# Kernel optimization log

Measured on AMD Instinct MI355X. Metric: run time of the kernel, lower is better.

Reference implementation:

```python
import jax, jax.numpy as jnp
import numpy as np

LRELU_SLOPE = 0.1  # correlate_operator uses F.leaky_relu_(corr, 0.1)


def _conv2d(x, w, b):
    # x: [B,Ci,H,W], w: [Co,Ci,kh,kw], stride 1, padding SAME (=padding=1 for 3x3)
    y = jax.lax.conv_general_dilated(x, w, (1, 1), 'SAME',
                                     dimension_numbers=('NCHW', 'OIHW', 'NCHW'))
    return y + b[None, :, None, None]


def correlate(x1, x2):
    # spatial_correlation_sample(x1, x2, kernel_size=3, patch_size=1, stride=1,
    # padding=1): with patch_size=1 the only displacement is (0,0), so the cost
    # volume is a 3x3 window sum of the per-pixel channel dot product.
    # Then divided by C and leaky_relu(0.1) as in correlate_operator.
    prod = jnp.sum(x1 * x2, axis=1, keepdims=True)  # [B,1,H,W]
    box = jnp.ones((1, 1, 3, 3), prod.dtype)
    corr = jax.lax.conv_general_dilated(prod, box, (1, 1), 'SAME',
                                        dimension_numbers=('NCHW', 'OIHW', 'NCHW'))
    corr = corr / x1.shape[1]
    return jnp.where(corr > 0, corr, LRELU_SLOPE * corr)


def deform_conv2d(x, offset, w):
    # mmcv DeformConv2d: kernel 3x3, stride 1, pad 1, dilation 1, deform_groups=1,
    # bias=False. offset: [B, 2*kh*kw, H, W], per kernel tap k: (dy_k, dx_k).
    B, Cin, H, W = x.shape
    O, _, kh, kw = w.shape
    K = kh * kw
    off = offset.reshape(B, K, 2, H, W)
    dy, dx = off[:, :, 0], off[:, :, 1]  # [B,K,H,W]
    ky, kx = jnp.meshgrid(jnp.arange(kh), jnp.arange(kw), indexing='ij')
    # sampling position: p + p_k + offset_k (pad=1 cancels the kernel-center shift)
    y = jnp.arange(H, dtype=x.dtype)[None, None, :, None] \
        + (ky.reshape(-1) - kh // 2).astype(x.dtype)[None, :, None, None] + dy
    xx = jnp.arange(W, dtype=x.dtype)[None, None, None, :] \
        + (kx.reshape(-1) - kw // 2).astype(x.dtype)[None, :, None, None] + dx
    y0 = jnp.floor(y)
    x0 = jnp.floor(xx)
    wy = (y - y0)[:, None]   # [B,1,K,H,W]
    wx = (xx - x0)[:, None]
    y0i = y0.astype(jnp.int32)
    x0i = x0.astype(jnp.int32)
    xf = x.reshape(B, Cin, H * W)

    def gather(yi, xi):
        valid = (yi >= 0) & (yi < H) & (xi >= 0) & (xi < W)  # zero padding outside
        idx = jnp.clip(yi, 0, H - 1) * W + jnp.clip(xi, 0, W - 1)
        v = jnp.take_along_axis(xf, idx.reshape(B, 1, K * H * W), axis=2)
        return v.reshape(B, Cin, K, H, W) * valid.astype(x.dtype)[:, None]

    v00 = gather(y0i, x0i)
    v01 = gather(y0i, x0i + 1)
    v10 = gather(y0i + 1, x0i)
    v11 = gather(y0i + 1, x0i + 1)
    samp = (v00 * (1 - wy) * (1 - wx) + v01 * (1 - wy) * wx
            + v10 * wy * (1 - wx) + v11 * wy * wx)  # [B,Cin,K,H,W]
    return jnp.einsum('bckhw,ock->bohw', samp, w.reshape(O, Cin, K))


def setup_inputs() -> dict:
    key = jax.random.key(0)
    ks = jax.random.split(key, 10)
    B, C, H, W = 4, 256, 64, 64
    s = 0.02
    return {
        'x_ref': jax.random.normal(ks[0], (B, C, H, W), jnp.float32),
        'x_next': jax.random.normal(ks[1], (B, C, H, W), jnp.float32),
        'w1': jax.random.normal(ks[2], (256, 1, 3, 3), jnp.float32) * s,
        'b1': jax.random.normal(ks[3], (256,), jnp.float32) * s,
        'w2': jax.random.normal(ks[4], (256, 256, 3, 3), jnp.float32) * s,
        'b2': jax.random.normal(ks[5], (256,), jnp.float32) * s,
        'w3': jax.random.normal(ks[6], (18, 256, 3, 3), jnp.float32) * s,
        'b3': jax.random.normal(ks[7], (18,), jnp.float32) * s,
        'w_dcn': jax.random.normal(ks[8], (256, 256, 3, 3), jnp.float32) * s,
        'idx': 4,
    }


def reference(x_ref, x_next, w1, b1, w2, b2, w3, b3, w_dcn, idx):
    # idx=4 -> corr_patch_size=1 (consistent with conv1 in_channels)
    corr = correlate(x_next, x_ref)                      # [B,1,H,W]
    h = jax.nn.relu(_conv2d(corr, w1, b1))               # [B,256,H,W]
    h = jax.nn.relu(_conv2d(h, w2, b2))                  # [B,256,H,W]
    offset = jax.nn.relu(_conv2d(h, w3, b3))             # [B,18,H,W]
    x_ref_cal = jax.nn.relu(deform_conv2d(x_ref, offset, w_dcn))
    return 0.5 * (x_next + x_ref_cal)
```

## Files before the change

kernel.cpp:

```cpp
#include <hip/hip_runtime.h>

typedef __attribute__((ext_vector_type(8))) short short8v;
typedef __attribute__((ext_vector_type(4))) float f32x4;
typedef __attribute__((ext_vector_type(2))) float f32x2;
typedef __attribute__((ext_vector_type(4))) unsigned int u32x4;

constexpr int Bsz = 4;
constexpr int Hh = 64, Wwd = 64;
constexpr int HWp = Hh * Wwd;
constexpr int NPIX = Bsz * HWp;
constexpr int HH = 66;
constexpr int HPIX = HH * HH;
constexpr int Kdim = 2304;
constexpr int NSTEP = 36;

constexpr size_t B_H1H  = 0;
constexpr size_t HALO_BYTES = (size_t)Bsz * HPIX * 256 * 2;
constexpr size_t B_H2H  = B_H1H + HALO_BYTES;
constexpr size_t B_XTH  = B_H2H + HALO_BYTES;
constexpr size_t B_PROD = B_XTH + HALO_BYTES;
constexpr size_t B_OFFP = B_PROD + (size_t)NPIX * 4;
constexpr size_t B_WB2  = B_OFFP + (size_t)NPIX * 32 * 4;
constexpr size_t B_WBD  = B_WB2 + (size_t)256 * Kdim * 2;
constexpr size_t B_WB3  = B_WBD + (size_t)256 * Kdim * 2;

static __device__ __forceinline__ unsigned short f2bf(float f) {
    unsigned u = __builtin_bit_cast(unsigned, f);
    u += 0x7FFFu + ((u >> 16) & 1u);
    return (unsigned short)(u >> 16);
}
static __device__ __forceinline__ unsigned cvt_pk_bf16(float lo, float hi) {
    unsigned r;
    asm("v_cvt_pk_bf16_f32 %0, %1, %2" : "=v"(r) : "v"(lo), "v"(hi));
    return r;
}
static __device__ __forceinline__ f32x2 pk_mul(f32x2 a, f32x2 b) {
    f32x2 d;
    asm("v_pk_mul_f32 %0, %1, %2" : "=v"(d) : "v"(a), "v"(b));
    return d;
}
static __device__ __forceinline__ f32x2 pk_fma(f32x2 a, f32x2 b, f32x2 c) {
    f32x2 d;
    asm("v_pk_fma_f32 %0, %1, %2, %3" : "=v"(d) : "v"(a), "v"(b), "v"(c));
    return d;
}
static __device__ __forceinline__ f32x2 unpack2(unsigned u) {
    f32x2 v;
    v.x = __builtin_bit_cast(float, u << 16);
    v.y = __builtin_bit_cast(float, u & 0xFFFF0000u);
    return v;
}
static __device__ __forceinline__ int swz(int u) {
    return (((u & 7) ^ ((u >> 3) & 7)) << 3);
}

__global__ void k_zero_ring(unsigned short* h1h, unsigned short* h2h, unsigned short* xth,
                            float* prod) {
    int blk = blockIdx.x;
    if (blk >= 3120) {
        unsigned* p = (unsigned*)prod + (size_t)(blk - 3120) * 128 + threadIdx.x;
        *p = 0;
        return;
    }
    int img = blk / 260;
    int rp = blk - img * 260;
    int buf = img >> 2, b = img & 3;
    int y, x;
    if (rp < 66) { y = 0; x = rp; }
    else if (rp < 132) { y = 65; x = rp - 66; }
    else { int s2 = rp - 132; y = 1 + (s2 >> 1); x = (s2 & 1) * 65; }
    unsigned short* base = (buf == 0) ? h1h : (buf == 1) ? h2h : xth;
    unsigned* p = (unsigned*)(base + ((size_t)b * HPIX + y * HH + x) * 256);
    p[threadIdx.x] = 0;
}

__global__ void k_prodx(const float* __restrict__ xr, const float* __restrict__ xn,
                        unsigned short* __restrict__ xth, float* __restrict__ prod) {
    __shared__ float t[32][33];
    __shared__ float red[8][33];
    int b = blockIdx.z;
    int c0 = blockIdx.y * 32;
    int y = blockIdx.x >> 1, x0 = (blockIdx.x & 1) * 32;
    int tx = threadIdx.x, ty = threadIdx.y;
    float part = 0.f;
#pragma unroll
    for (int i = 0; i < 32; i += 8) {
        size_t idx = ((size_t)b * 256 + c0 + ty + i) * HWp + y * Wwd + x0 + tx;
        float vr = xr[idx];
        float vn = xn[idx];
        t[ty + i][tx] = vr;
        part = fmaf(vr, vn, part);
    }
    red[ty][tx] = part;
    __syncthreads();
#pragma unroll
    for (int i = 0; i < 32; i += 8)
        xth[((size_t)b * HPIX + (y + 1) * HH + (x0 + ty + i + 1)) * 256 + c0 + tx] =
            f2bf(t[tx][ty + i]);
    if (ty == 0) {
        float s = red[0][tx] + red[1][tx] + red[2][tx] + red[3][tx] +
                  red[4][tx] + red[5][tx] + red[6][tx] + red[7][tx];
        atomicAdd(&prod[b * HWp + y * Wwd + x0 + tx], s);
    }
}

__global__ __launch_bounds__(256) void k_conv1c(const float* __restrict__ prod,
                                                const float* __restrict__ w1,
                                                const float* __restrict__ b1,
                                                unsigned short* __restrict__ h1h) {
    __shared__ float pp[5][36];
    __shared__ float pt[3][34];
    int px0 = blockIdx.x * 32;
    int b = px0 >> 12, y = (px0 & 4095) >> 6, x0 = px0 & 63;
    int tid = threadIdx.x;
    if (tid < 180) {
        int i = tid / 36, j = tid - i * 36;
        int yy = y - 2 + i, xx = x0 - 2 + j;
        float v = 0.f;
        if (yy >= 0 && yy < Hh && xx >= 0 && xx < Wwd) v = prod[b * HWp + yy * Wwd + xx];
        pp[i][j] = v;
    }
    __syncthreads();
    if (tid < 102) {
        int i = tid / 34, j = tid - i * 34;
        int yy = y - 1 + i, xx = x0 - 1 + j;
        float v = 0.f;
        if (yy >= 0 && yy < Hh && xx >= 0 && xx < Wwd) {
            float s = pp[i][j]     + pp[i][j + 1]     + pp[i][j + 2] +
                      pp[i + 1][j] + pp[i + 1][j + 1] + pp[i + 1][j + 2] +
                      pp[i + 2][j] + pp[i + 2][j + 1] + pp[i + 2][j + 2];
            s *= (1.0f / 256.0f);
            v = (s > 0.f) ? s : 0.1f * s;
        }
        pt[i][j] = v;
    }
    float wl[9];
#pragma unroll
    for (int k = 0; k < 9; ++k) wl[k] = w1[tid * 9 + k];
    float bias = b1[tid];
    __syncthreads();
    for (int p = 0; p < 32; ++p) {
        float acc = bias;
#pragma unroll
        for (int ky = 0; ky < 3; ++ky)
#pragma unroll
            for (int kx = 0; kx < 3; ++kx) acc = fmaf(pt[ky][p + kx], wl[ky * 3 + kx], acc);
        acc = fmaxf(acc, 0.f);
        h1h[((size_t)b * HPIX + (y + 1) * HH + (x0 + p + 1)) * 256 + tid] = f2bf(acc);
    }
}

__global__ void k_packall(const float* __restrict__ w2, const float* __restrict__ wd,
                          const float* __restrict__ w3,
                          unsigned short* __restrict__ wb2f, unsigned short* __restrict__ wbdf,
                          unsigned short* __restrict__ wb3f) {
    int blk = blockIdx.x;
    if (blk < 4608) {
        const float* w = (blk < 2304) ? w2 : wd;
        unsigned short* out = (blk < 2304) ? wb2f : wbdf;
        int i = (blk % 2304) * 256 + threadIdx.x;
        int e = i & 7;
        int lane = (i >> 3) & 63;
        int mi = (i >> 9) & 1;
        int kf = (i >> 10) & 1;
        int rest = i >> 11;
        int s = rest % 36;
        int wv = rest / 36;
        int o = wv * 32 + mi * 16 + (lane & 15);
        int kk = s * 64 + (kf * 4 + (lane >> 4)) * 8 + e;
        int c = kk & 255, tap = kk >> 8;
        out[i] = f2bf(w[((size_t)o * 256 + c) * 9 + tap]);
    } else {
        int i = (blk - 4608) * 256 + threadIdx.x;
        int e = i & 7;
        int lane = (i >> 3) & 63;
        int oi = (i >> 9) & 1;
        int kf = (i >> 10) & 1;
        int s = i >> 11;
        int o = oi * 16 + (lane & 15);
        int kk = s * 64 + (kf * 4 + (lane >> 4)) * 8 + e;
        int c = kk & 255, tap = kk >> 8;
        float v = (o < 18) ? w3[((size_t)o * 256 + c) * 9 + tap] : 0.f;
        wb3f[i] = f2bf(v);
    }
}

__global__ __launch_bounds__(256) void k_conv2g(const unsigned short* __restrict__ h1h,
                                                const unsigned short* __restrict__ wbf,
                                                const float* __restrict__ bias,
                                                unsigned short* __restrict__ h2h) {
    __shared__ short S_s[4][64 * 64];
    const int tid = threadIdx.x;
    const int bid = blockIdx.x;
    const int lin = (bid & 7) * 64 + (bid >> 3);
    const int px0 = (lin >> 1) * 64;
    const int oblk = lin & 1;
    const int b = px0 >> 12;
    const unsigned short* hb = h1h + (size_t)b * HPIX * 256;
    const int pxl = tid >> 2;
    const int px = px0 + pxl;
    const int y = (px & 4095) >> 6, x = px & 63;
    const int u0 = (tid & 3) * 2;
    const int lane = tid & 63, wv = tid >> 6;
    const int ot = oblk * 4 + wv;
    const unsigned short* wfb = wbf + (size_t)ot * NSTEP * 2048 + lane * 8;
    const unsigned short* abase0 = hb + (size_t)((y + 1) * HH + (x + 1)) * 256 + u0 * 8;

    f32x4 acc[4][2] = {};
    u32x4 wA[2][4], wB[2][4];
    u32x4 aP[4], aQ[4];
    float bia[2];
#pragma unroll
    for (int oi = 0; oi < 2; ++oi) bia[oi] = bias[ot * 32 + oi * 16 + (lane & 15)];

    const int wr0 = pxl * 64 + ((u0 ^ (pxl & 7)) << 3);
    const int wr1 = pxl * 64 + (((u0 + 1) ^ (pxl & 7)) << 3);

    auto WLOAD = [&](int s, u32x4 (&wreg)[4]) {
#pragma unroll
        for (int f = 0; f < 4; ++f)
            wreg[f] = *(const u32x4*)(wfb + ((size_t)s * 4 + f) * 512);
    };
    auto ALOAD = [&](int s, u32x4& a0, u32x4& a1) {
        int tap = s >> 2, chunk = s & 3;
        int aoff = ((tap / 3 - 1) * HH + (tap % 3 - 1)) * 256 + chunk * 64;
        a0 = *(const u32x4*)(abase0 + aoff);
        a1 = *(const u32x4*)(abase0 + aoff + 8);
    };

    {
        u32x4 a0, a1, a2, a3;
        ALOAD(0, a0, a1);
        ALOAD(1, a2, a3);
        WLOAD(0, wA[0]);
        WLOAD(1, wA[1]);
        *(u32x4*)&S_s[0][wr0] = a0;
        *(u32x4*)&S_s[0][wr1] = a1;
        *(u32x4*)&S_s[1][wr0] = a2;
        *(u32x4*)&S_s[1][wr1] = a3;
        ALOAD(2, aP[0], aP[1]);
        ALOAD(3, aP[2], aP[3]);
        asm volatile("s_waitcnt lgkmcnt(0)" ::: "memory");
    }

    auto ITER2 = [&](int s, u32x4 (&wcur)[2][4], u32x4 (&wnxt)[2][4],
                     u32x4 (&aC)[4], u32x4 (&aN)[4], short* SBc, short* SBn) {
        __builtin_amdgcn_s_barrier();
        __builtin_amdgcn_sched_barrier(0);
        if (s + 2 < NSTEP) {
            *(u32x4*)&SBn[wr0] = aC[0];
            *(u32x4*)&SBn[wr1] = aC[1];
            *(u32x4*)&SBn[64 * 64 + wr0] = aC[2];
            *(u32x4*)&SBn[64 * 64 + wr1] = aC[3];
        }
        if (s + 4 < NSTEP) {
            ALOAD(s + 4, aN[0], aN[1]);
            ALOAD(s + 5, aN[2], aN[3]);
        }
        if (s + 2 < NSTEP) {
            WLOAD(s + 2, wnxt[0]);
            WLOAD(s + 3, wnxt[1]);
        }
#pragma unroll
        for (int half = 0; half < 2; ++half) {
            const short* SB = SBc + half * 64 * 64;
            short8v af[4][2];
#pragma unroll
            for (int pi = 0; pi < 4; ++pi) {
                int row = pi * 16 + (lane & 15);
#pragma unroll
                for (int kf = 0; kf < 2; ++kf) {
                    int c8 = kf * 4 + (lane >> 4);
                    af[pi][kf] = *(const short8v*)&SB[row * 64 + ((c8 ^ (row & 7)) << 3)];
                }
            }
            __builtin_amdgcn_s_setprio(1);
#pragma unroll
            for (int kf = 0; kf < 2; ++kf)
#pragma unroll
                for (int pi = 0; pi < 4; ++pi)
#pragma unroll
                    for (int oi = 0; oi < 2; ++oi)
                        acc[pi][oi] = __builtin_amdgcn_mfma_f32_16x16x32_bf16(
                            af[pi][kf], __builtin_bit_cast(short8v, wcur[half][kf * 2 + oi]),
                            acc[pi][oi], 0, 0, 0);
            __builtin_amdgcn_s_setprio(0);
        }
        asm volatile("s_waitcnt lgkmcnt(0)" ::: "memory");
    };

    for (int s4 = 0; s4 < NSTEP; s4 += 4) {
        ITER2(s4, wA, wB, aP, aQ, &S_s[0][0], &S_s[2][0]);
        ITER2(s4 + 2, wB, wA, aQ, aP, &S_s[2][0], &S_s[0][0]);
    }

#pragma unroll
    for (int pi = 0; pi < 4; ++pi) {
#pragma unroll
        for (int j = 0; j < 4; ++j) {
            int p2 = px0 + pi * 16 + (lane >> 4) * 4 + j;
            int yy = (p2 & 4095) >> 6, xx = p2 & 63;
            unsigned short* dst = h2h + ((size_t)b * HPIX + (yy + 1) * HH + (xx + 1)) * 256;
#pragma unroll
            for (int oi = 0; oi < 2; ++oi) {
                int o = ot * 32 + oi * 16 + (lane & 15);
                dst[o] = f2bf(fmaxf(acc[pi][oi][j] + bia[oi], 0.f));
            }
        }
    }
}

__global__ __launch_bounds__(256) void k_conv3g(const unsigned short* __restrict__ h2h,
                                                const unsigned short* __restrict__ wb3f,
                                                const float* __restrict__ bias,
                                                float* __restrict__ offp) {
    __shared__ short S_s[4][64 * 64];
    const int tid = threadIdx.x;
    const int bid = blockIdx.x;
    const int px0 = ((bid & 7) * 32 + (bid >> 3)) * 64;
    const int b = px0 >> 12;
    const unsigned short* hb = h2h + (size_t)b * HPIX * 256;
    const int pxl = tid >> 2;
    const int px = px0 + pxl;
    const int y = (px & 4095) >> 6, x = px & 63;
    const int u0 = (tid & 3) * 2;
    const int lane = tid & 63, wv = tid >> 6;
    const unsigned short* wfb = wb3f + lane * 8;
    const unsigned short* abase0 = hb + (size_t)((y + 1) * HH + (x + 1)) * 256 + u0 * 8;

    f32x4 acc[2] = {};
    u32x4 wA[2][4], wB[2][4];
    u32x4 aP[4], aQ[4];
    float bia[2];
#pragma unroll
    for (int oi = 0; oi < 2; ++oi) {
        int o = oi * 16 + (lane & 15);
        bia[oi] = (o < 18) ? bias[o] : 0.f;
    }

    const int wr0 = pxl * 64 + ((u0 ^ (pxl & 7)) << 3);
    const int wr1 = pxl * 64 + (((u0 + 1) ^ (pxl & 7)) << 3);

    auto WLOAD = [&](int s, u32x4 (&wreg)[4]) {
#pragma unroll
        for (int f = 0; f < 4; ++f)
            wreg[f] = *(const u32x4*)(wfb + ((size_t)s * 4 + f) * 512);
    };
    auto ALOAD = [&](int s, u32x4& a0, u32x4& a1) {
        int tap = s >> 2, chunk = s & 3;
        int aoff = ((tap / 3 - 1) * HH + (tap % 3 - 1)) * 256 + chunk * 64;
        a0 = *(const u32x4*)(abase0 + aoff);
        a1 = *(const u32x4*)(abase0 + aoff + 8);
    };

    {
        u32x4 a0, a1, a2, a3;
        ALOAD(0, a0, a1);
        ALOAD(1, a2, a3);
        WLOAD(0, wA[0]);
        WLOAD(1, wA[1]);
        *(u32x4*)&S_s[0][wr0] = a0;
        *(u32x4*)&S_s[0][wr1] = a1;
        *(u32x4*)&S_s[1][wr0] = a2;
        *(u32x4*)&S_s[1][wr1] = a3;
        ALOAD(2, aP[0], aP[1]);
        ALOAD(3, aP[2], aP[3]);
        asm volatile("s_waitcnt lgkmcnt(0)" ::: "memory");
    }

    auto ITER2 = [&](int s, u32x4 (&wcur)[2][4], u32x4 (&wnxt)[2][4],
                     u32x4 (&aC)[4], u32x4 (&aN)[4], short* SBc, short* SBn) {
        __builtin_amdgcn_s_barrier();
        __builtin_amdgcn_sched_barrier(0);
        if (s + 2 < NSTEP) {
            *(u32x4*)&SBn[wr0] = aC[0];
            *(u32x4*)&SBn[wr1] = aC[1];
            *(u32x4*)&SBn[64 * 64 + wr0] = aC[2];
            *(u32x4*)&SBn[64 * 64 + wr1] = aC[3];
        }
        if (s + 4 < NSTEP) {
            ALOAD(s + 4, aN[0], aN[1]);
            ALOAD(s + 5, aN[2], aN[3]);
        }
        if (s + 2 < NSTEP) {
            WLOAD(s + 2, wnxt[0]);
            WLOAD(s + 3, wnxt[1]);
        }
#pragma unroll
        for (int half = 0; half < 2; ++half) {
            const short* SB = SBc + half * 64 * 64;
            short8v af[2];
#pragma unroll
            for (int kf = 0; kf < 2; ++kf) {
                int row = wv * 16 + (lane & 15);
                int c8 = kf * 4 + (lane >> 4);
                af[kf] = *(const short8v*)&SB[row * 64 + ((c8 ^ (row & 7)) << 3)];
            }
            __builtin_amdgcn_s_setprio(1);
#pragma unroll
            for (int kf = 0; kf < 2; ++kf)
#pragma unroll
                for (int oi = 0; oi < 2; ++oi)
                    acc[oi] = __builtin_amdgcn_mfma_f32_16x16x32_bf16(
                        af[kf], __builtin_bit_cast(short8v, wcur[half][kf * 2 + oi]),
                        acc[oi], 0, 0, 0);
            __builtin_amdgcn_s_setprio(0);
        }
        asm volatile("s_waitcnt lgkmcnt(0)" ::: "memory");
    };

    for (int s4 = 0; s4 < NSTEP; s4 += 4) {
        ITER2(s4, wA, wB, aP, aQ, &S_s[0][0], &S_s[2][0]);
        ITER2(s4 + 2, wB, wA, aQ, aP, &S_s[2][0], &S_s[0][0]);
    }

#pragma unroll
    for (int j = 0; j < 4; ++j) {
        int p2 = px0 + wv * 16 + (lane >> 4) * 4 + j;
#pragma unroll
        for (int oi = 0; oi < 2; ++oi) {
            int o = oi * 16 + (lane & 15);
            offp[(size_t)p2 * 32 + o] = fmaxf(acc[oi][j] + bia[oi], 0.f);
        }
    }
}

__global__ __launch_bounds__(512) void k_dcng(const unsigned short* __restrict__ xth,
                                              const float* __restrict__ offp,
                                              const unsigned short* __restrict__ wbf,
                                              const float* __restrict__ xn,
                                              float* __restrict__ out) {
    __shared__ short S_s[4][64 * 64];
    const int tid = threadIdx.x;
    const int bid = blockIdx.x;
    const int px0 = ((bid & 7) * 32 + (bid >> 3)) * 64;
    const int b = px0 >> 12;
    const unsigned short* xb = xth + (size_t)b * HPIX * 256;
    const int pxl = tid >> 3;
    const int px = px0 + pxl;
    const int y = (px & 4095) >> 6, x = px & 63;
    const int u0 = tid & 7;
    const int lane = tid & 63, wv = tid >> 6;
    const unsigned short* wfb = wbf + (size_t)wv * NSTEP * 2048 + lane * 8;
    const float2* offv = (const float2*)offp;

    f32x4 acc[2][4] = {};
    u32x4 wA[2][4], wB[2][4];
    u32x4 g[2][4];
    const int wr0 = pxl * 64 + ((u0 ^ (pxl & 7)) << 3);

    const unsigned short* pcorner[4];
    f32x2 wpair[4];
    float2 offn;

    auto SETUP = [&](int tap, float dyo, float dxo) {
        int ky = tap / 3 - 1, kx = tap % 3 - 1;
        float ypos = (float)(y + ky) + dyo;
        float xpos = (float)(x + kx) + dxo;
        float y0f = floorf(ypos), x0f = floorf(xpos);
        float wy = ypos - y0f, wx = xpos - x0f;
        int y0 = (int)y0f, x0 = (int)x0f;
        bool y0v = (y0 >= 0) && (y0 < Hh), y1v = (y0 + 1 >= 0) && (y0 + 1 < Hh);
        bool x0v = (x0 >= 0) && (x0 < Wwd), x1v = (x0 + 1 >= 0) && (x0 + 1 < Wwd);
        int hy0 = min(max(y0, -1), 64) + 1, hy1 = min(max(y0 + 1, -1), 64) + 1;
        int hx0 = min(max(x0, -1), 64) + 1, hx1 = min(max(x0 + 1, -1), 64) + 1;
        float w0 = (1.f - wy) * (1.f - wx) * (float)(y0v && x0v);
        float w1 = (1.f - wy) * wx * (float)(y0v && x1v);
        float w2 = wy * (1.f - wx) * (float)(y1v && x0v);
        float w3 = wy * wx * (float)(y1v && x1v);
        wpair[0] = (f32x2){w0, w0};
        wpair[1] = (f32x2){w1, w1};
        wpair[2] = (f32x2){w2, w2};
        wpair[3] = (f32x2){w3, w3};
        pcorner[0] = xb + (size_t)((hy0 * HH + hx0) * 256) + u0 * 8;
        pcorner[1] = xb + (size_t)((hy0 * HH + hx1) * 256) + u0 * 8;
        pcorner[2] = xb + (size_t)((hy1 * HH + hx0) * 256) + u0 * 8;
        pcorner[3] = xb + (size_t)((hy1 * HH + hx1) * 256) + u0 * 8;
    };
    auto WLOAD = [&](int s, u32x4 (&wreg)[4]) {
#pragma unroll
        for (int f = 0; f < 4; ++f)
            wreg[f] = *(const u32x4*)(wfb + ((size_t)s * 4 + f) * 512);
    };
    auto GISSUE = [&](int s, u32x4 (&gr)[4]) {
        const int nco = (s & 3) * 64;
#pragma unroll
        for (int c = 0; c < 4; ++c) gr[c] = *(const u32x4*)(pcorner[c] + nco);
    };
    auto COMBINE_WRITE = [&](u32x4 (&gr)[4], short* SBn) {
        u32x4 res;
#pragma unroll
        for (int qd = 0; qd < 4; ++qd) {
            f32x2 a = pk_mul(unpack2(gr[0][qd]), wpair[0]);
            a = pk_fma(unpack2(gr[1][qd]), wpair[1], a);
            a = pk_fma(unpack2(gr[2][qd]), wpair[2], a);
            a = pk_fma(unpack2(gr[3][qd]), wpair[3], a);
            res[qd] = cvt_pk_bf16(a.x, a.y);
        }
        *(u32x4*)&SBn[wr0] = res;
    };

    {
        float2 o0 = offv[(size_t)px * 16];
        SETUP(0, o0.x, o0.y);
        u32x4 g0[4], g1[4];
        GISSUE(0, g0);
        GISSUE(1, g1);
        WLOAD(0, wA[0]);
        WLOAD(1, wA[1]);
        COMBINE_WRITE(g0, &S_s[0][0]);
        COMBINE_WRITE(g1, &S_s[1][0]);
        GISSUE(2, g[0]);
        GISSUE(3, g[1]);
        offn = offv[(size_t)px * 16 + 1];
        asm volatile("s_waitcnt lgkmcnt(0)" ::: "memory");
    }

    auto ITER2 = [&](int s, u32x4 (&wcur)[2][4], u32x4 (&wnxt)[2][4], short* SBc, short* SBn) {
        __builtin_amdgcn_s_barrier();
        __builtin_amdgcn_sched_barrier(0);
        if (s + 2 < NSTEP) {
            COMBINE_WRITE(g[0], SBn);
            COMBINE_WRITE(g[1], SBn + 64 * 64);
        }
        if ((s & 3) == 0 && s + 4 < NSTEP)
            SETUP((s + 4) >> 2, offn.x, offn.y);
        if ((s & 3) == 2 && ((s + 8) >> 2) < 9)
            offn = offv[(size_t)px * 16 + ((s + 8) >> 2)];
        if (s + 4 < NSTEP) {
            GISSUE(s + 4, g[0]);
            GISSUE(s + 5, g[1]);
        }
        if (s + 2 < NSTEP) {
            WLOAD(s + 2, wnxt[0]);
            WLOAD(s + 3, wnxt[1]);
        }
#pragma unroll
        for (int half = 0; half < 2; ++half) {
            const short* SB = SBc + half * 64 * 64;
            short8v sf[4][2];
#pragma unroll
            for (int ni = 0; ni < 4; ++ni) {
                int row = ni * 16 + (lane & 15);
#pragma unroll
                for (int kf = 0; kf < 2; ++kf) {
                    int c8 = kf * 4 + (lane >> 4);
                    sf[ni][kf] = *(const short8v*)&SB[row * 64 + ((c8 ^ (row & 7)) << 3)];
                }
            }
            __builtin_amdgcn_s_setprio(1);
#pragma unroll
            for (int kf = 0; kf < 2; ++kf)
#pragma unroll
                for (int mi = 0; mi < 2; ++mi)
#pragma unroll
                    for (int ni = 0; ni < 4; ++ni)
                        acc[mi][ni] = __builtin_amdgcn_mfma_f32_16x16x32_bf16(
                            __builtin_bit_cast(short8v, wcur[half][kf * 2 + mi]), sf[ni][kf],
                            acc[mi][ni], 0, 0, 0);
            __builtin_amdgcn_s_setprio(0);
        }
        asm volatile("s_waitcnt lgkmcnt(0)" ::: "memory");
    };

    for (int s4 = 0; s4 < NSTEP; s4 += 4) {
        ITER2(s4, wA, wB, &S_s[0][0], &S_s[2][0]);
        ITER2(s4 + 2, wB, wA, &S_s[2][0], &S_s[0][0]);
    }

#pragma unroll
    for (int mi = 0; mi < 2; ++mi) {
        int o = wv * 32 + mi * 16 + (lane >> 4) * 4;
#pragma unroll
        for (int j = 0; j < 4; ++j) {
            size_t rowbase = ((size_t)b * 256 + o + j) * HWp;
#pragma unroll
            for (int ni = 0; ni < 4; ++ni) {
                int p2 = (px0 + ni * 16 + (lane & 15)) & 4095;
                size_t idx = rowbase + p2;
                out[idx] = 0.5f * (xn[idx] + fmaxf(acc[mi][ni][j], 0.f));
            }
        }
    }
}

extern "C" void kernel_launch(void* const* d_in, const int* in_sizes, int n_in,
                              void* d_out, int out_size, void* d_ws, size_t ws_size,
                              hipStream_t stream) {
    const float* x_ref  = (const float*)d_in[0];
    const float* x_next = (const float*)d_in[1];
    const float* w1 = (const float*)d_in[2];
    const float* b1 = (const float*)d_in[3];
    const float* w2 = (const float*)d_in[4];
    const float* b2 = (const float*)d_in[5];
    const float* w3 = (const float*)d_in[6];
    const float* b3 = (const float*)d_in[7];
    const float* wd = (const float*)d_in[8];
    float* out = (float*)d_out;
    char* ws = (char*)d_ws;

    unsigned short* h1h = (unsigned short*)(ws + B_H1H);
    unsigned short* h2h = (unsigned short*)(ws + B_H2H);
    unsigned short* xth = (unsigned short*)(ws + B_XTH);
    float* prod = (float*)(ws + B_PROD);
    float* offp = (float*)(ws + B_OFFP);
    unsigned short* wb2f = (unsigned short*)(ws + B_WB2);
    unsigned short* wbdf = (unsigned short*)(ws + B_WBD);
    unsigned short* wb3f = (unsigned short*)(ws + B_WB3);

    k_zero_ring<<<3120 + 128, 128, 0, stream>>>(h1h, h2h, xth, prod);
    k_prodx<<<dim3(128, 8, Bsz), dim3(32, 8), 0, stream>>>(x_ref, x_next, xth, prod);
    k_packall<<<4896, 256, 0, stream>>>(w2, wd, w3, wb2f, wbdf, wb3f);
    k_conv1c<<<NPIX / 32, 256, 0, stream>>>(prod, w1, b1, h1h);
    k_conv2g<<<512, 256, 0, stream>>>(h1h, wb2f, b2, h2h);
    k_conv3g<<<256, 256, 0, stream>>>(h2h, wb3f, b3, offp);
    k_dcng<<<256, 512, 0, stream>>>(xth, offp, wbdf, x_next, out);
}
```

Measured before the change: 97.49 us.

## Split deformable conv K dimension across two blocks and combine partials

The deformable-conv GEMM kernel now launches 512 blocks instead of 256. Each block handles half of the 36 K-steps for its 64-pixel tile and writes raw fp32 partial sums to one of two workspace buffers, one of which reuses the h1 halo region. A new elementwise kernel adds the two partials, applies ReLU and averages with x_next. The aim is to fill more compute units on the device, at the cost of extra partial-sum traffic and one more kernel launch.

```diff
diff --git a/kernel.cpp b/kernel.cpp
--- a/kernel.cpp
+++ b/kernel.cpp
@@ -23,6 +23,7 @@
 constexpr size_t B_WB2  = B_OFFP + (size_t)NPIX * 32 * 4;
 constexpr size_t B_WBD  = B_WB2 + (size_t)256 * Kdim * 2;
 constexpr size_t B_WB3  = B_WBD + (size_t)256 * Kdim * 2;
+constexpr size_t B_PARTB = B_WB3 + (size_t)73728 * 2;
 
 static __device__ __forceinline__ unsigned short f2bf(float f) {
     unsigned u = __builtin_bit_cast(unsigned, f);
@@ -428,12 +429,16 @@
 __global__ __launch_bounds__(512) void k_dcng(const unsigned short* __restrict__ xth,
                                               const float* __restrict__ offp,
                                               const unsigned short* __restrict__ wbf,
-                                              const float* __restrict__ xn,
-                                              float* __restrict__ out) {
+                                              float* __restrict__ partA,
+                                              float* __restrict__ partB) {
     __shared__ short S_s[4][64 * 64];
     const int tid = threadIdx.x;
     const int bid = blockIdx.x;
-    const int px0 = ((bid & 7) * 32 + (bid >> 3)) * 64;
+    const int lin = (bid & 7) * 64 + (bid >> 3);
+    const int px0 = (lin >> 1) * 64;
+    const int kb = lin & 1;
+    const int S0 = kb * 18, SEND = S0 + 18;
+    float* part = kb ? partB : partA;
     const int b = px0 >> 12;
     const unsigned short* xb = xth + (size_t)b * HPIX * 256;
     const int pxl = tid >> 3;
@@ -501,37 +506,43 @@
     };
 
     {
-        float2 o0 = offv[(size_t)px * 16];
-        SETUP(0, o0.x, o0.y);
+        int tap0 = S0 >> 2;
+        float2 o0 = offv[(size_t)px * 16 + tap0];
+        SETUP(tap0, o0.x, o0.y);
         u32x4 g0[4], g1[4];
-        GISSUE(0, g0);
-        GISSUE(1, g1);
-        WLOAD(0, wA[0]);
-        WLOAD(1, wA[1]);
+        GISSUE(S0, g0);
+        GISSUE(S0 + 1, g1);
+        WLOAD(S0, wA[0]);
+        WLOAD(S0 + 1, wA[1]);
         COMBINE_WRITE(g0, &S_s[0][0]);
         COMBINE_WRITE(g1, &S_s[1][0]);
-        GISSUE(2, g[0]);
-        GISSUE(3, g[1]);
-        offn = offv[(size_t)px * 16 + 1];
+        if ((S0 & 3) == 2) {
+            float2 o1 = offv[(size_t)px * 16 + tap0 + 1];
+            SETUP(tap0 + 1, o1.x, o1.y);
+        }
+        GISSUE(S0 + 2, g[0]);
+        GISSUE(S0 + 3, g[1]);
+        int tn = (S0 >> 2) + 1;
+        offn = offv[(size_t)px * 16 + (tn <= 8 ? tn : 8)];
         asm volatile("s_waitcnt lgkmcnt(0)" ::: "memory");
     }
 
     auto ITER2 = [&](int s, u32x4 (&wcur)[2][4], u32x4 (&wnxt)[2][4], short* SBc, short* SBn) {
         __builtin_amdgcn_s_barrier();
         __builtin_amdgcn_sched_barrier(0);
-        if (s + 2 < NSTEP) {
+        if (s + 2 < SEND) {
             COMBINE_WRITE(g[0], SBn);
             COMBINE_WRITE(g[1], SBn + 64 * 64);
         }
-        if ((s & 3) == 0 && s + 4 < NSTEP)
+        if ((s & 3) == 0 && s + 4 < SEND)
             SETUP((s + 4) >> 2, offn.x, offn.y);
         if ((s & 3) == 2 && ((s + 8) >> 2) < 9)
             offn = offv[(size_t)px * 16 + ((s + 8) >> 2)];
-        if (s + 4 < NSTEP) {
+        if (s + 4 < SEND) {
             GISSUE(s + 4, g[0]);
             GISSUE(s + 5, g[1]);
         }
-        if (s + 2 < NSTEP) {
+        if (s + 2 < SEND) {
             WLOAD(s + 2, wnxt[0]);
             WLOAD(s + 3, wnxt[1]);
         }
@@ -563,10 +574,11 @@
         asm volatile("s_waitcnt lgkmcnt(0)" ::: "memory");
     };
 
-    for (int s4 = 0; s4 < NSTEP; s4 += 4) {
+    for (int s4 = S0; s4 < S0 + 16; s4 += 4) {
         ITER2(s4, wA, wB, &S_s[0][0], &S_s[2][0]);
         ITER2(s4 + 2, wB, wA, &S_s[2][0], &S_s[0][0]);
     }
+    ITER2(S0 + 16, wA, wB, &S_s[0][0], &S_s[2][0]);
 
 #pragma unroll
     for (int mi = 0; mi < 2; ++mi) {
@@ -577,11 +589,23 @@
 #pragma unroll
             for (int ni = 0; ni < 4; ++ni) {
                 int p2 = (px0 + ni * 16 + (lane & 15)) & 4095;
-                size_t idx = rowbase + p2;
-                out[idx] = 0.5f * (xn[idx] + fmaxf(acc[mi][ni][j], 0.f));
+                part[rowbase + p2] = acc[mi][ni][j];
             }
         }
     }
+}
+
+__global__ void k_comb(const float* __restrict__ pA, const float* __restrict__ pB,
+                       const float* __restrict__ xn, float* __restrict__ out) {
+    int i = blockIdx.x * 256 + threadIdx.x;
+    f32x4 a = ((const f32x4*)pA)[i];
+    f32x4 bb = ((const f32x4*)pB)[i];
+    f32x4 n = ((const f32x4*)xn)[i];
+    f32x4 r;
+#pragma unroll
+    for (int j = 0; j < 4; ++j)
+        r[j] = 0.5f * (n[j] + fmaxf(a[j] + bb[j], 0.f));
+    ((f32x4*)out)[i] = r;
 }
 
 extern "C" void kernel_launch(void* const* d_in, const int* in_sizes, int n_in,
@@ -607,6 +631,8 @@
     unsigned short* wb2f = (unsigned short*)(ws + B_WB2);
     unsigned short* wbdf = (unsigned short*)(ws + B_WBD);
     unsigned short* wb3f = (unsigned short*)(ws + B_WB3);
+    float* partA = (float*)(ws + B_H1H);
+    float* partB = (float*)(ws + B_PARTB);
 
     k_zero_ring<<<3120 + 128, 128, 0, stream>>>(h1h, h2h, xth, prod);
     k_prodx<<<dim3(128, 8, Bsz), dim3(32, 8), 0, stream>>>(x_ref, x_next, xth, prod);
@@ -614,5 +640,6 @@
     k_conv1c<<<NPIX / 32, 256, 0, stream>>>(prod, w1, b1, h1h);
     k_conv2g<<<512, 256, 0, stream>>>(h1h, wb2f, b2, h2h);
     k_conv3g<<<256, 256, 0, stream>>>(h2h, wb3f, b3, offp);
-    k_dcng<<<256, 512, 0, stream>>>(xth, offp, wbdf, x_next, out);
-}
+    k_dcng<<<512, 512, 0, stream>>>(xth, offp, wbdf, partA, partB);
+    k_comb<<<4096, 256, 0, stream>>>(partA, partB, x_next, out);
+}
```

After: 109.4 us. 1.12x slower.
